# Optimization experiments

Measured on AMD Instinct MI355X. Metric: run time of the kernel, lower is better.

## Reference

```python
import jax, jax.numpy as jnp
import numpy as np
from jax import lax

DIM = 96
HEADS = 3
EPS = 1e-12


def conv1x1(x, w):
    # x: [b,c,h,w], w: [o,c]
    return jnp.einsum('bchw,oc->bohw', x, w)


def dwconv3(x, w):
    # depthwise 3x3, SAME padding. w: [C,1,3,3]
    C = x.shape[1]
    return lax.conv_general_dilated(
        x, w, window_strides=(1, 1), padding='SAME',
        feature_group_count=C,
        dimension_numbers=('NCHW', 'OIHW', 'NCHW'))


def channel_attn(q, kv, temperature):
    # q: [b,C,h,w], kv: [b,2C,h,w], temperature: [heads,1,1]
    k, v = jnp.split(kv, 2, axis=1)
    b, C, h, w = q.shape
    c = C // HEADS
    r = lambda x: x.reshape(b, HEADS, c, h * w)
    q, k, v = r(q), r(k), r(v)
    # L2-normalize along the (h*w) axis (torch F.normalize semantics)
    qn = q / jnp.maximum(jnp.linalg.norm(q, axis=-1, keepdims=True), EPS)
    kn = k / jnp.maximum(jnp.linalg.norm(k, axis=-1, keepdims=True), EPS)
    attn = jnp.einsum('bhcn,bhdn->bhcd', qn, kn) * temperature  # [b,heads,c,c]
    attn = jax.nn.softmax(attn, axis=-1)
    out = jnp.einsum('bhcd,bhdn->bhcn', attn, v)
    return out.reshape(b, C, h, w)


def setup_inputs() -> dict:
    key = jax.random.key(0)
    ks = jax.random.split(key, 16)
    d = DIM
    s = lambda fan: 1.0 / np.sqrt(fan)
    inp = {
        'low': jax.random.normal(ks[0], (2, d, 256, 256), jnp.float32),
        'high': jax.random.normal(ks[1], (2, d, 256, 256), jnp.float32),
        'temperature': jnp.ones((HEADS, 1, 1), jnp.float32),
        'qc_w': jax.random.normal(ks[2], (d, d), jnp.float32) * s(d),
        'qdw_c_w': jax.random.normal(ks[3], (d, 1, 3, 3), jnp.float32) * s(9),
        'kvc_w': jax.random.normal(ks[4], (2 * d, d), jnp.float32) * s(d),
        'kvdw_c_w': jax.random.normal(ks[5], (2 * d, 1, 3, 3), jnp.float32) * s(9),
        'qt_w': jax.random.normal(ks[6], (d, d), jnp.float32) * s(d),
        'qdw_t_w': jax.random.normal(ks[7], (d, 1, 3, 3), jnp.float32) * s(9),
        'kvt_w': jax.random.normal(ks[8], (2 * d, d), jnp.float32) * s(d),
        'kvdw_t_w': jax.random.normal(ks[9], (2 * d, 1, 3, 3), jnp.float32) * s(9),
        'po_c_w': jax.random.normal(ks[10], (d, d), jnp.float32) * s(d),
        'po_t_w': jax.random.normal(ks[11], (d, d), jnp.float32) * s(d),
        'concat_w': jax.random.normal(ks[12], (d, 2 * d), jnp.float32) * s(2 * d),
        'concat_b': jax.random.normal(ks[13], (d,), jnp.float32) * s(2 * d),
    }
    return inp


def reference(low, high, temperature, qc_w, qdw_c_w, kvc_w, kvdw_c_w,
              qt_w, qdw_t_w, kvt_w, kvdw_t_w, po_c_w, po_t_w,
              concat_w, concat_b):
    q_c = dwconv3(conv1x1(high, qc_w), qdw_c_w)
    kv_c = dwconv3(conv1x1(high, kvc_w), kvdw_c_w)
    q_t = dwconv3(conv1x1(low, qt_w), qdw_t_w)
    kv_t = dwconv3(conv1x1(low, kvt_w), kvdw_t_w)
    out_c = conv1x1(channel_attn(q_c, kv_t, temperature), po_c_w)
    out_t = conv1x1(channel_attn(q_t, kv_c, temperature), po_t_w)
    out = jnp.concatenate([out_c, out_t], axis=1)
    out = conv1x1(out, concat_w) + concat_b[None, :, None, None]
    return out
```

## Files before the change

### kernel.cpp

```cpp
#include <hip/hip_runtime.h>
#include <hip/hip_bf16.h>

#define HW 65536

typedef __attribute__((ext_vector_type(8))) short short8;
typedef __attribute__((ext_vector_type(4))) float f32x4;

static __device__ __forceinline__ ushort f2bf(float f) {
    union { float f; unsigned u; } v; v.f = f;
    unsigned u = v.u;
    unsigned r = (u + 0x7fffu + ((u >> 16) & 1u)) >> 16;
    return (ushort)r;
}
static __device__ __forceinline__ float bf2f(ushort u) {
    union { unsigned u; float f; } v; v.u = ((unsigned)u) << 16; return v.f;
}
static __device__ __forceinline__ unsigned pk2(float a, float b) {
    __hip_bfloat162 h = __float22bfloat162_rn(make_float2(a, b));
    union { __hip_bfloat162 h; unsigned u; } c; c.h = h; return c.u;
}
static __device__ __forceinline__ f32x4 mfma16(short8 a, short8 b, f32x4 c) {
    return __builtin_amdgcn_mfma_f32_16x16x32_bf16(a, b, c, 0, 0, 0);
}
union U8 { short8 s; unsigned u[4]; };

__global__ __launch_bounds__(256) void prep_kernel(
        const float* __restrict__ qc, const float* __restrict__ kvc,
        const float* __restrict__ qt, const float* __restrict__ kvt,
        const float* __restrict__ cw, const float* __restrict__ poc, const float* __restrict__ pot,
        ushort* __restrict__ Wc, ushort* __restrict__ Wt,
        float* __restrict__ W1, float* __restrict__ W2) {
    int bx = blockIdx.x, tid = threadIdx.x;
    if (bx == 0) {
        for (int idx = tid; idx < 288 * 96; idx += 256) {
            Wc[idx] = f2bf(idx < 96 * 96 ? qc[idx] : kvc[idx - 96 * 96]);
            Wt[idx] = f2bf(idx < 96 * 96 ? qt[idx] : kvt[idx - 96 * 96]);
        }
    } else {
        int idx = (bx - 1) * 256 + tid;
        int sel = idx < 9216 ? 0 : 1;
        int i = sel ? idx - 9216 : idx;
        int o = i / 96, m = i % 96;
        const float* po = sel ? pot : poc;
        float acc = 0.f;
        for (int p = 0; p < 96; ++p)
            acc += cw[o * 192 + sel * 96 + p] * po[p * 96 + m];
        (sel ? W2 : W1)[i] = acc;
    }
}

__global__ __launch_bounds__(256) void conv_kernel(const float* __restrict__ X,
                                                   const ushort* __restrict__ W,
                                                   ushort* __restrict__ Y) {
    __shared__ ushort xs[96 * 130];
    __shared__ ushort ybuf[2][128 * 18];
    int tid = threadIdx.x;
    int n0 = blockIdx.x * 128;
    int b = blockIdx.y;
    const float* Xb = X + (size_t)b * 96 * HW + n0;
    #pragma unroll
    for (int i = 0; i < 12; ++i) {
        int idx = tid + i * 256;
        int nq = idx & 31, k = idx >> 5;
        float4 v = *(const float4*)(Xb + (size_t)k * HW + 4 * nq);
        unsigned* dst = (unsigned*)&xs[k * 130 + 4 * nq];
        dst[0] = pk2(v.x, v.y);
        dst[1] = pk2(v.z, v.w);
    }
    __syncthreads();
    int wave = tid >> 6, lane = tid & 63, lr = lane & 15, lg = lane >> 4;
    short8 bf[2][3];
    #pragma unroll
    for (int nt = 0; nt < 2; ++nt) {
        int n = wave * 32 + nt * 16 + lr;
        #pragma unroll
        for (int kk = 0; kk < 3; ++kk) {
            int kb = kk * 32 + lg * 8;
            U8 t;
            #pragma unroll
            for (int j = 0; j < 4; ++j) {
                unsigned e0 = xs[(kb + 2 * j) * 130 + n];
                unsigned e1 = xs[(kb + 2 * j + 1) * 130 + n];
                t.u[j] = e0 | (e1 << 16);
            }
            bf[nt][kk] = t.s;
        }
    }
    ushort* Yb = Y + (size_t)b * 288 * HW + n0;
    for (int mt = 0; mt < 18; ++mt) {
        f32x4 acc0 = {0.f, 0.f, 0.f, 0.f}, acc1 = {0.f, 0.f, 0.f, 0.f};
        #pragma unroll
        for (int kk = 0; kk < 3; ++kk) {
            short8 a = *(const short8*)&W[(size_t)(mt * 16 + lr) * 96 + kk * 32 + lg * 8];
            acc0 = mfma16(a, bf[0][kk], acc0);
            acc1 = mfma16(a, bf[1][kk], acc1);
        }
        ushort* yb = ybuf[mt & 1];
        {
            unsigned* d0 = (unsigned*)&yb[(wave * 32 + lr) * 18 + lg * 4];
            d0[0] = pk2(acc0[0], acc0[1]);
            d0[1] = pk2(acc0[2], acc0[3]);
            unsigned* d1 = (unsigned*)&yb[(wave * 32 + 16 + lr) * 18 + lg * 4];
            d1[0] = pk2(acc1[0], acc1[1]);
            d1[1] = pk2(acc1[2], acc1[3]);
        }
        __syncthreads();
        {
            int o = tid >> 4, g = tid & 15;
            U8 t;
            #pragma unroll
            for (int j = 0; j < 4; ++j) {
                unsigned e0 = yb[(8 * g + 2 * j) * 18 + o];
                unsigned e1 = yb[(8 * g + 2 * j + 1) * 18 + o];
                t.u[j] = e0 | (e1 << 16);
            }
            *(short8*)&Yb[(size_t)(mt * 16 + o) * HW + 8 * g] = t.s;
        }
    }
}

__global__ __launch_bounds__(256) void dw_kernel(const ushort* __restrict__ Y,
                                                 const float* __restrict__ qdw,
                                                 const float* __restrict__ kvdw,
                                                 ushort* __restrict__ QKV) {
    __shared__ ushort tile[34 * 256];
    int tid = threadIdx.x;
    int ch = blockIdx.y % 288, b = blockIdx.y / 288;
    int r0 = blockIdx.x * 32;
    const float* w = (ch < 96) ? (qdw + ch * 9) : (kvdw + (ch - 96) * 9);
    float w00 = w[0], w01 = w[1], w02 = w[2], w10 = w[3], w11 = w[4],
          w12 = w[5], w20 = w[6], w21 = w[7], w22 = w[8];
    const ushort* src = Y + (size_t)(b * 288 + ch) * HW;
    #pragma unroll
    for (int i = 0; i < 5; ++i) {
        int idx = tid + i * 256;
        if (idx < 34 * 32) {
            int row = idx >> 5, g = idx & 31;
            int gr = r0 - 1 + row;
            short8 v;
            if (gr >= 0 && gr < 256) v = *(const short8*)(src + gr * 256 + 8 * g);
            else v = (short8){0, 0, 0, 0, 0, 0, 0, 0};
            *(short8*)&tile[row * 256 + 8 * g] = v;
        }
    }
    __syncthreads();
    int wave = tid >> 6, lane = tid & 63;
    float rows[3][6];
    #define LOADROW(LROW, D)                                                 \
    {                                                                        \
        ushort4 t4 = *(const ushort4*)&tile[(LROW) * 256 + 4 * lane];        \
        float c0 = bf2f(t4.x), c1 = bf2f(t4.y), c2 = bf2f(t4.z), c3 = bf2f(t4.w); \
        float lft = __shfl(c3, lane - 1);                                    \
        float rgt = __shfl(c0, lane + 1);                                    \
        if (lane == 0) lft = 0.f;                                            \
        if (lane == 63) rgt = 0.f;                                           \
        D[0] = lft; D[1] = c0; D[2] = c1; D[3] = c2; D[4] = c3; D[5] = rgt;  \
    }
    LOADROW(wave * 8 + 0, rows[0]);
    LOADROW(wave * 8 + 1, rows[1]);
    ushort* dst = QKV + (size_t)(b * 288 + ch) * HW;
    #pragma unroll
    for (int orow = 0; orow < 8; ++orow) {
        LOADROW(wave * 8 + orow + 2, rows[(orow + 2) % 3]);
        float* ra = rows[orow % 3];
        float* rb = rows[(orow + 1) % 3];
        float* rc = rows[(orow + 2) % 3];
        float acc[4];
        #pragma unroll
        for (int j = 0; j < 4; ++j)
            acc[j] = w00 * ra[j] + w01 * ra[j + 1] + w02 * ra[j + 2]
                   + w10 * rb[j] + w11 * rb[j + 1] + w12 * rb[j + 2]
                   + w20 * rc[j] + w21 * rc[j + 1] + w22 * rc[j + 2];
        uint2 pv;
        pv.x = pk2(acc[0], acc[1]);
        pv.y = pk2(acc[2], acc[3]);
        *(uint2*)&dst[(r0 + wave * 8 + orow) * 256 + 4 * lane] = pv;
    }
    #undef LOADROW
}

__global__ __launch_bounds__(256) void gram_kernel(const ushort* __restrict__ QKVc,
                                                   const ushort* __restrict__ QKVt,
                                                   float* __restrict__ G,
                                                   float* __restrict__ SSQ) {
    __shared__ float Gp[4][32][32];
    int tid = threadIdx.x, wave = tid >> 6, lane = tid & 63;
    int lr = lane & 15, lg = lane >> 4;
    int code = blockIdx.y;
    int a = code / 6, b = (code % 6) / 3, h = code % 3;
    const ushort* qsrc = (a == 0) ? QKVc : QKVt;
    const ushort* ksrc = (a == 0) ? QKVt : QKVc;
    const ushort* qrow0 = qsrc + (size_t)(b * 288 + 32 * h + lr) * HW;
    const ushort* krow0 = ksrc + (size_t)(b * 288 + 96 + 32 * h + lr) * HW;
    f32x4 acc[2][2], aqq[2], akk[2];
    #pragma unroll
    for (int i = 0; i < 2; ++i) {
        aqq[i] = (f32x4){0.f, 0.f, 0.f, 0.f};
        akk[i] = (f32x4){0.f, 0.f, 0.f, 0.f};
        #pragma unroll
        for (int j = 0; j < 2; ++j) acc[i][j] = (f32x4){0.f, 0.f, 0.f, 0.f};
    }
    for (int s = wave; s < 32; s += 4) {
        int n = blockIdx.x * 1024 + s * 32 + lg * 8;
        short8 aq[2], bk[2];
        aq[0] = *(const short8*)(qrow0 + n);
        aq[1] = *(const short8*)(qrow0 + (size_t)16 * HW + n);
        bk[0] = *(const short8*)(krow0 + n);
        bk[1] = *(const short8*)(krow0 + (size_t)16 * HW + n);
        acc[0][0] = mfma16(aq[0], bk[0], acc[0][0]);
        acc[0][1] = mfma16(aq[0], bk[1], acc[0][1]);
        acc[1][0] = mfma16(aq[1], bk[0], acc[1][0]);
        acc[1][1] = mfma16(aq[1], bk[1], acc[1][1]);
        aqq[0] = mfma16(aq[0], aq[0], aqq[0]);
        aqq[1] = mfma16(aq[1], aq[1], aqq[1]);
        akk[0] = mfma16(bk[0], bk[0], akk[0]);
        akk[1] = mfma16(bk[1], bk[1], akk[1]);
    }
    #pragma unroll
    for (int i = 0; i < 2; ++i)
        #pragma unroll
        for (int j = 0; j < 2; ++j)
            #pragma unroll
            for (int r = 0; r < 4; ++r)
                Gp[wave][i * 16 + lg * 4 + r][j * 16 + lr] = acc[i][j][r];
    __syncthreads();
    float* Gout = G + (size_t)code * 1024;
    for (int idx = tid; idx < 1024; idx += 256) {
        float ssum = 0.f;
        #pragma unroll
        for (int wv = 0; wv < 4; ++wv) ssum += (&Gp[wv][0][0])[idx];
        atomicAdd(&Gout[idx], ssum);
    }
    int qbase = ((a * 2 + b) * 2 + 0) * 96 + 32 * h;
    int kbase = ((a * 2 + b) * 2 + 1) * 96 + 32 * h;
    #pragma unroll
    for (int i = 0; i < 2; ++i)
        #pragma unroll
        for (int r = 0; r < 4; ++r)
            if (lr == lg * 4 + r) {
                atomicAdd(&SSQ[qbase + i * 16 + lr], aqq[i][r]);
                atomicAdd(&SSQ[kbase + i * 16 + lr], akk[i][r]);
            }
}

__global__ __launch_bounds__(256) void attn_kernel(const float* __restrict__ G,
                                                   const float* __restrict__ SSQ,
                                                   const float* __restrict__ temperature,
                                                   const float* __restrict__ W1,
                                                   const float* __restrict__ W2,
                                                   ushort* __restrict__ Mcat) {
    __shared__ float nq[32], nk[32], A[32][32];
    int tid = threadIdx.x;
    int code = blockIdx.x;
    int a = code / 6, b = (code % 6) / 3, h = code % 3;
    if (tid < 32)
        nq[tid] = fmaxf(sqrtf(fmaxf(SSQ[((a * 2 + b) * 2 + 0) * 96 + 32 * h + tid], 0.f)), 1e-12f);
    else if (tid < 64)
        nk[tid - 32] = fmaxf(sqrtf(fmaxf(SSQ[((a * 2 + b) * 2 + 1) * 96 + 32 * h + (tid - 32)], 0.f)), 1e-12f);
    __syncthreads();
    if (tid < 32) {
        const float* g = G + (size_t)code * 1024 + tid * 32;
        float t = temperature[h];
        float lgv[32];
        float inq = t / nq[tid];
        float mx = -1e30f;
        #pragma unroll
        for (int j = 0; j < 32; ++j) { lgv[j] = g[j] * inq / nk[j]; mx = fmaxf(mx, lgv[j]); }
        float ssum = 0.f;
        #pragma unroll
        for (int j = 0; j < 32; ++j) { lgv[j] = expf(lgv[j] - mx); ssum += lgv[j]; }
        float inv = 1.f / ssum;
        #pragma unroll
        for (int j = 0; j < 32; ++j) A[tid][j] = lgv[j] * inv;
    }
    __syncthreads();
    const float* Wm = (a == 0) ? W1 : W2;
    for (int idx = tid; idx < 96 * 32; idx += 256) {
        int o = idx >> 5, d = idx & 31;
        float acc = 0.f;
        #pragma unroll
        for (int i = 0; i < 32; ++i)
            acc += Wm[o * 96 + 32 * h + i] * A[i][d];
        Mcat[(size_t)(b * 96 + o) * 192 + a * 96 + 32 * h + d] = f2bf(acc);
    }
}

__global__ __launch_bounds__(256) void final_kernel(const ushort* __restrict__ QKVc,
                                                    const ushort* __restrict__ QKVt,
                                                    const ushort* __restrict__ Mcat,
                                                    const float* __restrict__ bias,
                                                    float* __restrict__ out) {
    __shared__ ushort vs[192 * 130];
    __shared__ float obuf[2][16 * 132];
    int tid = threadIdx.x;
    int n0 = blockIdx.x * 128, b = blockIdx.y;
    #pragma unroll
    for (int i = 0; i < 12; ++i) {
        int idx = tid + i * 256;
        int g = idx & 15, d = idx >> 4;
        const ushort* sp = (d < 96) ? (QKVt + (size_t)(b * 288 + 192 + d) * HW)
                                    : (QKVc + (size_t)(b * 288 + 192 + (d - 96)) * HW);
        U8 t;
        t.s = *(const short8*)(sp + n0 + 8 * g);
        unsigned* dst = (unsigned*)&vs[d * 130 + 8 * g];
        dst[0] = t.u[0]; dst[1] = t.u[1]; dst[2] = t.u[2]; dst[3] = t.u[3];
    }
    __syncthreads();
    int wave = tid >> 6, lane = tid & 63, lr = lane & 15, lg = lane >> 4;
    short8 bf[2][6];
    #pragma unroll
    for (int nt = 0; nt < 2; ++nt) {
        int n = wave * 32 + nt * 16 + lr;
        #pragma unroll
        for (int kk = 0; kk < 6; ++kk) {
            int kb = kk * 32 + lg * 8;
            U8 t;
            #pragma unroll
            for (int j = 0; j < 4; ++j) {
                unsigned e0 = vs[(kb + 2 * j) * 130 + n];
                unsigned e1 = vs[(kb + 2 * j + 1) * 130 + n];
                t.u[j] = e0 | (e1 << 16);
            }
            bf[nt][kk] = t.s;
        }
    }
    float* outb = out + (size_t)b * 96 * HW + n0;
    for (int mt = 0; mt < 6; ++mt) {
        f32x4 acc0 = {0.f, 0.f, 0.f, 0.f}, acc1 = {0.f, 0.f, 0.f, 0.f};
        #pragma unroll
        for (int kk = 0; kk < 6; ++kk) {
            short8 a = *(const short8*)&Mcat[(size_t)(b * 96 + mt * 16 + lr) * 192 + kk * 32 + lg * 8];
            acc0 = mfma16(a, bf[0][kk], acc0);
            acc1 = mfma16(a, bf[1][kk], acc1);
        }
        float* ob_ = obuf[mt & 1];
        #pragma unroll
        for (int r = 0; r < 4; ++r) {
            ob_[(lg * 4 + r) * 132 + wave * 32 + lr]      = acc0[r];
            ob_[(lg * 4 + r) * 132 + wave * 32 + 16 + lr] = acc1[r];
        }
        __syncthreads();
        #pragma unroll
        for (int p = 0; p < 2; ++p) {
            int flat = tid + p * 256;
            int row = flat >> 5, q = flat & 31;
            float4 v = *(const float4*)&ob_[row * 132 + 4 * q];
            float bb = bias[mt * 16 + row];
            v.x += bb; v.y += bb; v.z += bb; v.w += bb;
            *(float4*)&outb[(size_t)(mt * 16 + row) * HW + 4 * q] = v;
        }
    }
}

extern "C" void kernel_launch(void* const* d_in, const int* in_sizes, int n_in,
                              void* d_out, int out_size, void* d_ws, size_t ws_size,
                              hipStream_t stream) {
    const float* low    = (const float*)d_in[0];
    const float* high   = (const float*)d_in[1];
    const float* temp   = (const float*)d_in[2];
    const float* qc_w   = (const float*)d_in[3];
    const float* qdw_c  = (const float*)d_in[4];
    const float* kvc_w  = (const float*)d_in[5];
    const float* kvdw_c = (const float*)d_in[6];
    const float* qt_w   = (const float*)d_in[7];
    const float* qdw_t  = (const float*)d_in[8];
    const float* kvt_w  = (const float*)d_in[9];
    const float* kvdw_t = (const float*)d_in[10];
    const float* po_c   = (const float*)d_in[11];
    const float* po_t   = (const float*)d_in[12];
    const float* cw     = (const float*)d_in[13];
    const float* cb     = (const float*)d_in[14];
    float* out = (float*)d_out;

    char* ws = (char*)d_ws;
    const size_t SY = (size_t)2 * 288 * HW * 2;
    ushort* Y    = (ushort*)(ws);
    ushort* QKVc = (ushort*)(ws + SY);
    ushort* QKVt = (ushort*)(ws + 2 * SY);
    char* p = ws + 3 * SY;
    ushort* Wc = (ushort*)p; p += 288 * 96 * 2;
    ushort* Wt = (ushort*)p; p += 288 * 96 * 2;
    float* W1  = (float*)p;  p += 96 * 96 * 4;
    float* W2  = (float*)p;  p += 96 * 96 * 4;
    float* G   = (float*)p;  p += 12 * 1024 * 4;
    float* SSQ = (float*)p;  p += 8 * 96 * 4;
    ushort* Mcat = (ushort*)p; p += 2 * 96 * 192 * 2;
    if ((size_t)(p - ws) > ws_size) return;

    hipMemsetAsync(G, 0, 12 * 1024 * 4 + 8 * 96 * 4, stream);
    prep_kernel<<<73, 256, 0, stream>>>(qc_w, kvc_w, qt_w, kvt_w, cw, po_c, po_t, Wc, Wt, W1, W2);
    conv_kernel<<<dim3(512, 2), 256, 0, stream>>>(high, Wc, Y);
    dw_kernel<<<dim3(8, 576), 256, 0, stream>>>(Y, qdw_c, kvdw_c, QKVc);
    conv_kernel<<<dim3(512, 2), 256, 0, stream>>>(low, Wt, Y);
    dw_kernel<<<dim3(8, 576), 256, 0, stream>>>(Y, qdw_t, kvdw_t, QKVt);
    gram_kernel<<<dim3(64, 12), 256, 0, stream>>>(QKVc, QKVt, G, SSQ);
    attn_kernel<<<12, 256, 0, stream>>>(G, SSQ, temp, W1, W2, Mcat);
    final_kernel<<<dim3(512, 2), 256, 0, stream>>>(QKVc, QKVt, Mcat, cb, out);
}
```

Baseline: 250.4 us.

## Restructure convs to transposed MFMA, fuse SSQ into dwconv, deterministic gram partials

```diff
diff --git a/kernel.cpp b/kernel.cpp
--- a/kernel.cpp
+++ b/kernel.cpp
@@ -2,9 +2,11 @@
 #include <hip/hip_bf16.h>
 
 #define HW 65536
+#define GNS 64
 
 typedef __attribute__((ext_vector_type(8))) short short8;
 typedef __attribute__((ext_vector_type(4))) float f32x4;
+union U8 { short8 s; unsigned u[4]; ushort h[8]; };
 
 static __device__ __forceinline__ ushort f2bf(float f) {
     union { float f; unsigned u; } v; v.f = f;
@@ -22,7 +24,6 @@
 static __device__ __forceinline__ f32x4 mfma16(short8 a, short8 b, f32x4 c) {
     return __builtin_amdgcn_mfma_f32_16x16x32_bf16(a, b, c, 0, 0, 0);
 }
-union U8 { short8 s; unsigned u[4]; };
 
 __global__ __launch_bounds__(256) void prep_kernel(
         const float* __restrict__ qc, const float* __restrict__ kvc,
@@ -52,77 +53,55 @@
 __global__ __launch_bounds__(256) void conv_kernel(const float* __restrict__ X,
                                                    const ushort* __restrict__ W,
                                                    ushort* __restrict__ Y) {
-    __shared__ ushort xs[96 * 130];
-    __shared__ ushort ybuf[2][128 * 18];
+    __shared__ ushort xs[96][68];
     int tid = threadIdx.x;
-    int n0 = blockIdx.x * 128;
-    int b = blockIdx.y;
+    int n0 = blockIdx.x * 64, b = blockIdx.y;
     const float* Xb = X + (size_t)b * 96 * HW + n0;
     #pragma unroll
-    for (int i = 0; i < 12; ++i) {
+    for (int i = 0; i < 6; ++i) {
         int idx = tid + i * 256;
-        int nq = idx & 31, k = idx >> 5;
-        float4 v = *(const float4*)(Xb + (size_t)k * HW + 4 * nq);
-        unsigned* dst = (unsigned*)&xs[k * 130 + 4 * nq];
-        dst[0] = pk2(v.x, v.y);
-        dst[1] = pk2(v.z, v.w);
+        int ch = idx >> 4, g = idx & 15;
+        float4 v = *(const float4*)(Xb + (size_t)ch * HW + 4 * g);
+        unsigned* d = (unsigned*)&xs[ch][4 * g];
+        d[0] = pk2(v.x, v.y);
+        d[1] = pk2(v.z, v.w);
     }
     __syncthreads();
     int wave = tid >> 6, lane = tid & 63, lr = lane & 15, lg = lane >> 4;
-    short8 bf[2][3];
-    #pragma unroll
-    for (int nt = 0; nt < 2; ++nt) {
-        int n = wave * 32 + nt * 16 + lr;
+    int ncol = wave * 16 + lr;
+    short8 af[3];
+    #pragma unroll
+    for (int kk = 0; kk < 3; ++kk) {
+        int kb = kk * 32 + lg * 8;
+        U8 t;
+        #pragma unroll
+        for (int j = 0; j < 4; ++j) {
+            unsigned e0 = xs[kb + 2 * j][ncol];
+            unsigned e1 = xs[kb + 2 * j + 1][ncol];
+            t.u[j] = e0 | (e1 << 16);
+        }
+        af[kk] = t.s;
+    }
+    ushort* Yb = Y + (size_t)b * 288 * HW + n0 + wave * 16;
+    for (int mt = 0; mt < 18; ++mt) {
+        f32x4 acc = {0.f, 0.f, 0.f, 0.f};
         #pragma unroll
         for (int kk = 0; kk < 3; ++kk) {
-            int kb = kk * 32 + lg * 8;
-            U8 t;
-            #pragma unroll
-            for (int j = 0; j < 4; ++j) {
-                unsigned e0 = xs[(kb + 2 * j) * 130 + n];
-                unsigned e1 = xs[(kb + 2 * j + 1) * 130 + n];
-                t.u[j] = e0 | (e1 << 16);
-            }
-            bf[nt][kk] = t.s;
-        }
-    }
-    ushort* Yb = Y + (size_t)b * 288 * HW + n0;
-    for (int mt = 0; mt < 18; ++mt) {
-        f32x4 acc0 = {0.f, 0.f, 0.f, 0.f}, acc1 = {0.f, 0.f, 0.f, 0.f};
-        #pragma unroll
-        for (int kk = 0; kk < 3; ++kk) {
-            short8 a = *(const short8*)&W[(size_t)(mt * 16 + lr) * 96 + kk * 32 + lg * 8];
-            acc0 = mfma16(a, bf[0][kk], acc0);
-            acc1 = mfma16(a, bf[1][kk], acc1);
-        }
-        ushort* yb = ybuf[mt & 1];
-        {
-            unsigned* d0 = (unsigned*)&yb[(wave * 32 + lr) * 18 + lg * 4];
-            d0[0] = pk2(acc0[0], acc0[1]);
-            d0[1] = pk2(acc0[2], acc0[3]);
-            unsigned* d1 = (unsigned*)&yb[(wave * 32 + 16 + lr) * 18 + lg * 4];
-            d1[0] = pk2(acc1[0], acc1[1]);
-            d1[1] = pk2(acc1[2], acc1[3]);
-        }
-        __syncthreads();
-        {
-            int o = tid >> 4, g = tid & 15;
-            U8 t;
-            #pragma unroll
-            for (int j = 0; j < 4; ++j) {
-                unsigned e0 = yb[(8 * g + 2 * j) * 18 + o];
-                unsigned e1 = yb[(8 * g + 2 * j + 1) * 18 + o];
-                t.u[j] = e0 | (e1 << 16);
-            }
-            *(short8*)&Yb[(size_t)(mt * 16 + o) * HW + 8 * g] = t.s;
-        }
+            short8 wf = *(const short8*)&W[(size_t)(mt * 16 + lr) * 96 + kk * 32 + lg * 8];
+            acc = mfma16(af[kk], wf, acc);
+        }
+        uint2 pv;
+        pv.x = pk2(acc[0], acc[1]);
+        pv.y = pk2(acc[2], acc[3]);
+        *(uint2*)&Yb[(size_t)(mt * 16 + lr) * HW + lg * 4] = pv;
     }
 }
 
 __global__ __launch_bounds__(256) void dw_kernel(const ushort* __restrict__ Y,
                                                  const float* __restrict__ qdw,
                                                  const float* __restrict__ kvdw,
-                                                 ushort* __restrict__ QKV) {
+                                                 ushort* __restrict__ QKV,
+                                                 float* __restrict__ SSQ, int is_c) {
     __shared__ ushort tile[34 * 256];
     int tid = threadIdx.x;
     int ch = blockIdx.y % 288, b = blockIdx.y / 288;
@@ -146,6 +125,7 @@
     __syncthreads();
     int wave = tid >> 6, lane = tid & 63;
     float rows[3][6];
+    float ssq = 0.f;
     #define LOADROW(LROW, D)                                                 \
     {                                                                        \
         ushort4 t4 = *(const ushort4*)&tile[(LROW) * 256 + 4 * lane];        \
@@ -167,22 +147,35 @@
         float* rc = rows[(orow + 2) % 3];
         float acc[4];
         #pragma unroll
-        for (int j = 0; j < 4; ++j)
+        for (int j = 0; j < 4; ++j) {
             acc[j] = w00 * ra[j] + w01 * ra[j + 1] + w02 * ra[j + 2]
                    + w10 * rb[j] + w11 * rb[j + 1] + w12 * rb[j + 2]
                    + w20 * rc[j] + w21 * rc[j + 1] + w22 * rc[j + 2];
+            ssq += acc[j] * acc[j];
+        }
         uint2 pv;
         pv.x = pk2(acc[0], acc[1]);
         pv.y = pk2(acc[2], acc[3]);
         *(uint2*)&dst[(r0 + wave * 8 + orow) * 256 + 4 * lane] = pv;
     }
     #undef LOADROW
+    if (ch < 192) {
+        #pragma unroll
+        for (int off = 1; off < 64; off <<= 1) ssq += __shfl_xor(ssq, off);
+        if (lane == 0) {
+            int t_ = ch >= 96;
+            int chq = t_ ? ch - 96 : ch;
+            int a_ = is_c ? t_ : (1 - t_);
+            atomicAdd(&SSQ[((a_ * 2 + b) * 2 + t_) * 96 + chq], ssq);
+        }
+    }
 }
 
 __global__ __launch_bounds__(256) void gram_kernel(const ushort* __restrict__ QKVc,
                                                    const ushort* __restrict__ QKVt,
-                                                   float* __restrict__ G,
-                                                   float* __restrict__ SSQ) {
+                                                   float* __restrict__ Gpart) {
+    __shared__ ushort qs[32 * 256];
+    __shared__ ushort ks2[32 * 256];
     __shared__ float Gp[4][32][32];
     int tid = threadIdx.x, wave = tid >> 6, lane = tid & 63;
     int lr = lane & 15, lg = lane >> 4;
@@ -190,31 +183,38 @@
     int a = code / 6, b = (code % 6) / 3, h = code % 3;
     const ushort* qsrc = (a == 0) ? QKVc : QKVt;
     const ushort* ksrc = (a == 0) ? QKVt : QKVc;
-    const ushort* qrow0 = qsrc + (size_t)(b * 288 + 32 * h + lr) * HW;
-    const ushort* krow0 = ksrc + (size_t)(b * 288 + 96 + 32 * h + lr) * HW;
-    f32x4 acc[2][2], aqq[2], akk[2];
-    #pragma unroll
-    for (int i = 0; i < 2; ++i) {
-        aqq[i] = (f32x4){0.f, 0.f, 0.f, 0.f};
-        akk[i] = (f32x4){0.f, 0.f, 0.f, 0.f};
+    const ushort* qb = qsrc + (size_t)(b * 288 + 32 * h) * HW + blockIdx.x * 1024;
+    const ushort* kb = ksrc + (size_t)(b * 288 + 96 + 32 * h) * HW + blockIdx.x * 1024;
+    f32x4 acc[2][2];
+    #pragma unroll
+    for (int i = 0; i < 2; ++i)
         #pragma unroll
         for (int j = 0; j < 2; ++j) acc[i][j] = (f32x4){0.f, 0.f, 0.f, 0.f};
-    }
-    for (int s = wave; s < 32; s += 4) {
-        int n = blockIdx.x * 1024 + s * 32 + lg * 8;
-        short8 aq[2], bk[2];
-        aq[0] = *(const short8*)(qrow0 + n);
-        aq[1] = *(const short8*)(qrow0 + (size_t)16 * HW + n);
-        bk[0] = *(const short8*)(krow0 + n);
-        bk[1] = *(const short8*)(krow0 + (size_t)16 * HW + n);
-        acc[0][0] = mfma16(aq[0], bk[0], acc[0][0]);
-        acc[0][1] = mfma16(aq[0], bk[1], acc[0][1]);
-        acc[1][0] = mfma16(aq[1], bk[0], acc[1][0]);
-        acc[1][1] = mfma16(aq[1], bk[1], acc[1][1]);
-        aqq[0] = mfma16(aq[0], aq[0], aqq[0]);
-        aqq[1] = mfma16(aq[1], aq[1], aqq[1]);
-        akk[0] = mfma16(bk[0], bk[0], akk[0]);
-        akk[1] = mfma16(bk[1], bk[1], akk[1]);
+    for (int ph = 0; ph < 4; ++ph) {
+        int noff = ph * 256;
+        #pragma unroll
+        for (int i = 0; i < 4; ++i) {
+            int idx = tid + i * 256;
+            int row = idx >> 5, g = idx & 31;
+            int col = (g * 8) ^ ((row & 7) << 3);
+            *(short8*)&qs[row * 256 + col] = *(const short8*)(qb + (size_t)row * HW + noff + 8 * g);
+            *(short8*)&ks2[row * 256 + col] = *(const short8*)(kb + (size_t)row * HW + noff + 8 * g);
+        }
+        __syncthreads();
+        #pragma unroll
+        for (int j = 0; j < 2; ++j) {
+            int ks_ = wave * 2 + j;
+            int c0 = (ks_ * 32 + lg * 8) ^ ((lr & 7) << 3);
+            short8 a0 = *(const short8*)&qs[lr * 256 + c0];
+            short8 a1 = *(const short8*)&qs[(16 + lr) * 256 + c0];
+            short8 b0 = *(const short8*)&ks2[lr * 256 + c0];
+            short8 b1 = *(const short8*)&ks2[(16 + lr) * 256 + c0];
+            acc[0][0] = mfma16(a0, b0, acc[0][0]);
+            acc[0][1] = mfma16(a0, b1, acc[0][1]);
+            acc[1][0] = mfma16(a1, b0, acc[1][0]);
+            acc[1][1] = mfma16(a1, b1, acc[1][1]);
+        }
+        __syncthreads();
     }
     #pragma unroll
     for (int i = 0; i < 2; ++i)
@@ -224,48 +224,46 @@
             for (int r = 0; r < 4; ++r)
                 Gp[wave][i * 16 + lg * 4 + r][j * 16 + lr] = acc[i][j][r];
     __syncthreads();
-    float* Gout = G + (size_t)code * 1024;
+    float* Gout = Gpart + ((size_t)code * GNS + blockIdx.x) * 1024;
     for (int idx = tid; idx < 1024; idx += 256) {
         float ssum = 0.f;
         #pragma unroll
         for (int wv = 0; wv < 4; ++wv) ssum += (&Gp[wv][0][0])[idx];
-        atomicAdd(&Gout[idx], ssum);
-    }
-    int qbase = ((a * 2 + b) * 2 + 0) * 96 + 32 * h;
-    int kbase = ((a * 2 + b) * 2 + 1) * 96 + 32 * h;
-    #pragma unroll
-    for (int i = 0; i < 2; ++i)
-        #pragma unroll
-        for (int r = 0; r < 4; ++r)
-            if (lr == lg * 4 + r) {
-                atomicAdd(&SSQ[qbase + i * 16 + lr], aqq[i][r]);
-                atomicAdd(&SSQ[kbase + i * 16 + lr], akk[i][r]);
-            }
-}
-
-__global__ __launch_bounds__(256) void attn_kernel(const float* __restrict__ G,
+        Gout[idx] = ssum;
+    }
+}
+
+__global__ __launch_bounds__(256) void attn_kernel(const float* __restrict__ Gpart,
                                                    const float* __restrict__ SSQ,
                                                    const float* __restrict__ temperature,
                                                    const float* __restrict__ W1,
                                                    const float* __restrict__ W2,
                                                    ushort* __restrict__ Mcat) {
+    __shared__ float Gs[1024];
     __shared__ float nq[32], nk[32], A[32][32];
     int tid = threadIdx.x;
     int code = blockIdx.x;
     int a = code / 6, b = (code % 6) / 3, h = code % 3;
+    const float* gp = Gpart + (size_t)code * GNS * 1024;
+    #pragma unroll
+    for (int j = 0; j < 4; ++j) {
+        int idx = tid + j * 256;
+        float s = 0.f;
+        for (int p = 0; p < GNS; ++p) s += gp[(size_t)p * 1024 + idx];
+        Gs[idx] = s;
+    }
     if (tid < 32)
         nq[tid] = fmaxf(sqrtf(fmaxf(SSQ[((a * 2 + b) * 2 + 0) * 96 + 32 * h + tid], 0.f)), 1e-12f);
     else if (tid < 64)
         nk[tid - 32] = fmaxf(sqrtf(fmaxf(SSQ[((a * 2 + b) * 2 + 1) * 96 + 32 * h + (tid - 32)], 0.f)), 1e-12f);
     __syncthreads();
     if (tid < 32) {
-        const float* g = G + (size_t)code * 1024 + tid * 32;
         float t = temperature[h];
         float lgv[32];
         float inq = t / nq[tid];
         float mx = -1e30f;
         #pragma unroll
-        for (int j = 0; j < 32; ++j) { lgv[j] = g[j] * inq / nk[j]; mx = fmaxf(mx, lgv[j]); }
+        for (int j = 0; j < 32; ++j) { lgv[j] = Gs[tid * 32 + j] * inq / nk[j]; mx = fmaxf(mx, lgv[j]); }
         float ssum = 0.f;
         #pragma unroll
         for (int j = 0; j < 32; ++j) { lgv[j] = expf(lgv[j] - mx); ssum += lgv[j]; }
@@ -290,65 +288,48 @@
                                                     const ushort* __restrict__ Mcat,
                                                     const float* __restrict__ bias,
                                                     float* __restrict__ out) {
-    __shared__ ushort vs[192 * 130];
-    __shared__ float obuf[2][16 * 132];
+    __shared__ ushort vs[192][68];
     int tid = threadIdx.x;
-    int n0 = blockIdx.x * 128, b = blockIdx.y;
-    #pragma unroll
-    for (int i = 0; i < 12; ++i) {
+    int n0 = blockIdx.x * 64, b = blockIdx.y;
+    #pragma unroll
+    for (int i = 0; i < 6; ++i) {
         int idx = tid + i * 256;
-        int g = idx & 15, d = idx >> 4;
+        int d = idx >> 3, g = idx & 7;
         const ushort* sp = (d < 96) ? (QKVt + (size_t)(b * 288 + 192 + d) * HW)
                                     : (QKVc + (size_t)(b * 288 + 192 + (d - 96)) * HW);
         U8 t;
         t.s = *(const short8*)(sp + n0 + 8 * g);
-        unsigned* dst = (unsigned*)&vs[d * 130 + 8 * g];
+        unsigned* dst = (unsigned*)&vs[d][8 * g];
         dst[0] = t.u[0]; dst[1] = t.u[1]; dst[2] = t.u[2]; dst[3] = t.u[3];
     }
     __syncthreads();
     int wave = tid >> 6, lane = tid & 63, lr = lane & 15, lg = lane >> 4;
-    short8 bf[2][6];
-    #pragma unroll
-    for (int nt = 0; nt < 2; ++nt) {
-        int n = wave * 32 + nt * 16 + lr;
+    int ncol = wave * 16 + lr;
+    short8 vf[6];
+    #pragma unroll
+    for (int kk = 0; kk < 6; ++kk) {
+        int kbn = kk * 32 + lg * 8;
+        U8 t;
+        #pragma unroll
+        for (int j = 0; j < 4; ++j) {
+            unsigned e0 = vs[kbn + 2 * j][ncol];
+            unsigned e1 = vs[kbn + 2 * j + 1][ncol];
+            t.u[j] = e0 | (e1 << 16);
+        }
+        vf[kk] = t.s;
+    }
+    const ushort* Mb = Mcat + (size_t)b * 96 * 192;
+    float* outb = out + (size_t)b * 96 * HW + n0 + wave * 16;
+    for (int mt = 0; mt < 6; ++mt) {
+        f32x4 acc = {0.f, 0.f, 0.f, 0.f};
         #pragma unroll
         for (int kk = 0; kk < 6; ++kk) {
-            int kb = kk * 32 + lg * 8;
-            U8 t;
-            #pragma unroll
-            for (int j = 0; j < 4; ++j) {
-                unsigned e0 = vs[(kb + 2 * j) * 130 + n];
-                unsigned e1 = vs[(kb + 2 * j + 1) * 130 + n];
-                t.u[j] = e0 | (e1 << 16);
-            }
-            bf[nt][kk] = t.s;
-        }
-    }
-    float* outb = out + (size_t)b * 96 * HW + n0;
-    for (int mt = 0; mt < 6; ++mt) {
-        f32x4 acc0 = {0.f, 0.f, 0.f, 0.f}, acc1 = {0.f, 0.f, 0.f, 0.f};
-        #pragma unroll
-        for (int kk = 0; kk < 6; ++kk) {
-            short8 a = *(const short8*)&Mcat[(size_t)(b * 96 + mt * 16 + lr) * 192 + kk * 32 + lg * 8];
-            acc0 = mfma16(a, bf[0][kk], acc0);
-            acc1 = mfma16(a, bf[1][kk], acc1);
-        }
-        float* ob_ = obuf[mt & 1];
-        #pragma unroll
-        for (int r = 0; r < 4; ++r) {
-            ob_[(lg * 4 + r) * 132 + wave * 32 + lr]      = acc0[r];
-            ob_[(lg * 4 + r) * 132 + wave * 32 + 16 + lr] = acc1[r];
-        }
-        __syncthreads();
-        #pragma unroll
-        for (int p = 0; p < 2; ++p) {
-            int flat = tid + p * 256;
-            int row = flat >> 5, q = flat & 31;
-            float4 v = *(const float4*)&ob_[row * 132 + 4 * q];
-            float bb = bias[mt * 16 + row];
-            v.x += bb; v.y += bb; v.z += bb; v.w += bb;
-            *(float4*)&outb[(size_t)(mt * 16 + row) * HW + 4 * q] = v;
-        }
+            short8 mf = *(const short8*)&Mb[(size_t)(mt * 16 + lr) * 192 + kk * 32 + lg * 8];
+            acc = mfma16(vf[kk], mf, acc);
+        }
+        float bb = bias[mt * 16 + lr];
+        float4 v = make_float4(acc[0] + bb, acc[1] + bb, acc[2] + bb, acc[3] + bb);
+        *(float4*)&outb[(size_t)(mt * 16 + lr) * HW + lg * 4] = v;
     }
 }
 
@@ -377,6 +358,7 @@
     ushort* Y    = (ushort*)(ws);
     ushort* QKVc = (ushort*)(ws + SY);
     ushort* QKVt = (ushort*)(ws + 2 * SY);
+    float* Gpart = (float*)ws;
     char* p = ws + 3 * SY;
     ushort* Wc = (ushort*)p; p += 288 * 96 * 2;
     ushort* Wt = (ushort*)p; p += 288 * 96 * 2;
@@ -386,14 +368,15 @@
     float* SSQ = (float*)p;  p += 8 * 96 * 4;
     ushort* Mcat = (ushort*)p; p += 2 * 96 * 192 * 2;
     if ((size_t)(p - ws) > ws_size) return;
-
-    hipMemsetAsync(G, 0, 12 * 1024 * 4 + 8 * 96 * 4, stream);
+    (void)G;
+
+    hipMemsetAsync(SSQ, 0, 8 * 96 * 4, stream);
     prep_kernel<<<73, 256, 0, stream>>>(qc_w, kvc_w, qt_w, kvt_w, cw, po_c, po_t, Wc, Wt, W1, W2);
-    conv_kernel<<<dim3(512, 2), 256, 0, stream>>>(high, Wc, Y);
-    dw_kernel<<<dim3(8, 576), 256, 0, stream>>>(Y, qdw_c, kvdw_c, QKVc);
-    conv_kernel<<<dim3(512, 2), 256, 0, stream>>>(low, Wt, Y);
-    dw_kernel<<<dim3(8, 576), 256, 0, stream>>>(Y, qdw_t, kvdw_t, QKVt);
-    gram_kernel<<<dim3(64, 12), 256, 0, stream>>>(QKVc, QKVt, G, SSQ);
-    attn_kernel<<<12, 256, 0, stream>>>(G, SSQ, temp, W1, W2, Mcat);
-    final_kernel<<<dim3(512, 2), 256, 0, stream>>>(QKVc, QKVt, Mcat, cb, out);
-}
+    conv_kernel<<<dim3(1024, 2), 256, 0, stream>>>(high, Wc, Y);
+    dw_kernel<<<dim3(8, 576), 256, 0, stream>>>(Y, qdw_c, kvdw_c, QKVc, SSQ, 1);
+    conv_kernel<<<dim3(1024, 2), 256, 0, stream>>>(low, Wt, Y);
+    dw_kernel<<<dim3(8, 576), 256, 0, stream>>>(Y, qdw_t, kvdw_t, QKVt, SSQ, 0);
+    gram_kernel<<<dim3(GNS, 12), 256, 0, stream>>>(QKVc, QKVt, Gpart);
+    attn_kernel<<<12, 256, 0, stream>>>(Gpart, SSQ, temp, W1, W2, Mcat);
+    final_kernel<<<dim3(1024, 2), 256, 0, stream>>>(QKVc, QKVt, Mcat, cb, out);
+}
```

Result: slower. 318.9 us (+27.4%).
